# Kernel optimization log

Measured on AMD Instinct MI355X. Metric: run time of the kernel, lower is better.

The kernel has to match this reference:

```python
import jax, jax.numpy as jnp
import numpy as np

HIDDEN = 4096
N_HEADS = 32
N_KV_HEADS = 8
HEAD_DIM = HIDDEN // N_HEADS  # 128
ROPE_THETA = 10000.0
BATCH, SEQ = 2, 2048


def setup_inputs() -> dict:
    key = jax.random.key(0)
    ks = jax.random.split(key, 5)
    s = 0.02
    return {
        "hidden_states": jax.random.normal(ks[0], (BATCH, SEQ, HIDDEN), jnp.float32),
        "position_ids": jnp.broadcast_to(jnp.arange(SEQ, dtype=jnp.int32), (BATCH, SEQ)),
        "Wq": jax.random.normal(ks[1], (HIDDEN, HIDDEN), jnp.float32) * s,
        "Wk": jax.random.normal(ks[2], (N_KV_HEADS * HEAD_DIM, HIDDEN), jnp.float32) * s,
        "Wv": jax.random.normal(ks[3], (N_KV_HEADS * HEAD_DIM, HIDDEN), jnp.float32) * s,
        "Wo": jax.random.normal(ks[4], (HIDDEN, HIDDEN), jnp.float32) * s,
    }


def _rope_cos_sin(position_ids, dtype):
    # HF LlamaRotaryEmbedding: inv_freq over even dims, emb = concat(freqs, freqs)
    inv_freq = 1.0 / (ROPE_THETA ** (jnp.arange(0, HEAD_DIM, 2, dtype=jnp.float32) / HEAD_DIM))
    freqs = position_ids.astype(jnp.float32)[..., None] * inv_freq[None, None, :]  # [B,S,D/2]
    emb = jnp.concatenate([freqs, freqs], axis=-1)  # [B,S,D]
    return jnp.cos(emb).astype(dtype), jnp.sin(emb).astype(dtype)


def _rotate_half(x):
    x1, x2 = jnp.split(x, 2, axis=-1)
    return jnp.concatenate([-x2, x1], axis=-1)


def reference(hidden_states, position_ids, Wq, Wk, Wv, Wo):
    B, S, _ = hidden_states.shape
    dtype = hidden_states.dtype

    # QKV projections (nn.Linear: x @ W.T), reshape to [B, H, S, D]
    q = (hidden_states @ Wq.T).reshape(B, S, N_HEADS, HEAD_DIM).transpose(0, 2, 1, 3)
    k = (hidden_states @ Wk.T).reshape(B, S, N_KV_HEADS, HEAD_DIM).transpose(0, 2, 1, 3)
    v = (hidden_states @ Wv.T).reshape(B, S, N_KV_HEADS, HEAD_DIM).transpose(0, 2, 1, 3)

    # RoPE
    cos, sin = _rope_cos_sin(position_ids, dtype)  # [B,S,D]
    cos_b, sin_b = cos[:, None, :, :], sin[:, None, :, :]
    q = q * cos_b + _rotate_half(q) * sin_b
    k = k * cos_b + _rotate_half(k) * sin_b

    # GQA: group queries over shared kv heads instead of materializing repeat_kv
    groups = N_HEADS // N_KV_HEADS
    qg = q.reshape(B, N_KV_HEADS, groups, S, HEAD_DIM)

    scale = 1.0 / jnp.sqrt(jnp.asarray(HEAD_DIM, dtype=jnp.float32)).astype(dtype)
    scores = jnp.einsum('bkgqd,bkld->bkgql', qg, k) * scale  # [B,KV,G,S,S]

    causal = jnp.tril(jnp.ones((S, S), dtype=bool))
    scores = jnp.where(causal[None, None, None], scores, jnp.asarray(-jnp.inf, scores.dtype))
    probs = jax.nn.softmax(scores.astype(jnp.float32), axis=-1).astype(dtype)

    out = jnp.einsum('bkgql,bkld->bkgqd', probs, v)  # [B,KV,G,S,D]
    out = out.reshape(B, N_HEADS, S, HEAD_DIM).transpose(0, 2, 1, 3).reshape(B, S, HIDDEN)
    return out @ Wo.T
```

## Files before the change

### kernel.cpp

```cpp
#include <hip/hip_runtime.h>
#include <cstdint>
#include <cstddef>

typedef unsigned short u16;
typedef short bf16x8 __attribute__((ext_vector_type(8)));
typedef float f32x4 __attribute__((ext_vector_type(4)));

#define HIDDEN 4096
#define NH 32
#define NKV 8
#define HD 128
#define SEQL 2048
#define BATCH 2
#define NTOK (BATCH*SEQL)
#define QKVN (HIDDEN + 2*NKV*HD)

#define QKS 136

__device__ __forceinline__ u16 f2bf(float f){
    unsigned u = __float_as_uint(f);
    u += 0x7FFF + ((u >> 16) & 1);
    return (u16)(u >> 16);
}
__device__ __forceinline__ float bf2f(u16 h){
    return __uint_as_float(((unsigned)h) << 16);
}
__device__ __forceinline__ f32x4 zero4(){
    f32x4 z; z[0]=0.f; z[1]=0.f; z[2]=0.f; z[3]=0.f; return z;
}

typedef const unsigned int __attribute__((address_space(1)))* gas1_t;
typedef unsigned int __attribute__((address_space(3)))* las3_t;
__device__ __forceinline__ void gload_lds16(const u16* g, u16* l){
    __builtin_amdgcn_global_load_lds((gas1_t)g, (las3_t)l, 16, 0, 0);
}

__global__ __launch_bounds__(256) void cvt_kernel(const float* __restrict__ src,
                                                  u16* __restrict__ dst, int n4){
    int i = blockIdx.x * 256 + threadIdx.x;
    if (i < n4){
        float4 v = ((const float4*)src)[i];
        ushort4 o;
        o.x = f2bf(v.x); o.y = f2bf(v.y); o.z = f2bf(v.z); o.w = f2bf(v.w);
        ((ushort4*)dst)[i] = o;
    }
}

template<int OUT_BF16>
__global__ __launch_bounds__(256) void gemm_bt(const u16* __restrict__ A,
                                               const u16* __restrict__ B,
                                               void* __restrict__ Cp,
                                               int M, int N, int K){
    __shared__ __align__(16) u16 As[128*32];
    __shared__ __align__(16) u16 Bs[128*32];
    int tid = threadIdx.x;
    int wave = tid >> 6, lane = tid & 63, quad = lane >> 4, l16 = lane & 15;
    int wm = wave & 1, wn = wave >> 1;
    size_t row0 = (size_t)blockIdx.y * 128, col0 = (size_t)blockIdx.x * 128;

    f32x4 acc[4][4];
    #pragma unroll
    for (int i=0;i<4;i++)
        #pragma unroll
        for (int j=0;j<4;j++) acc[i][j] = zero4();

    int sg = tid >> 3, ss = tid & 7;
    int scc = ss ^ (sg & 7);
    int sr = sg * 2 + (scc >> 2), sc = scc & 3;
    const u16* Ag = A + (row0 + sr) * (size_t)K + sc * 8;
    const u16* Bg = B + (col0 + sr) * (size_t)K + sc * 8;
    u16* Asp = As + tid * 8;
    u16* Bsp = Bs + tid * 8;
    size_t skip = (size_t)64 * K;

    int fs = (((l16 & 1) * 4 + quad) ^ ((l16 >> 1) & 7)) * 8;
    int aoff = wm * 2048 + (l16 >> 1) * 64 + fs;
    int boff = wn * 2048 + (l16 >> 1) * 64 + fs;

    for (int k0 = 0; k0 < K; k0 += 32){
        gload_lds16(Ag + k0,        Asp);
        gload_lds16(Ag + k0 + skip, Asp + 2048);
        gload_lds16(Bg + k0,        Bsp);
        gload_lds16(Bg + k0 + skip, Bsp + 2048);
        __syncthreads();
        bf16x8 af[4], bfr[4];
        #pragma unroll
        for (int i=0;i<4;i++) af[i]  = *(const bf16x8*)(As + aoff + i*512);
        #pragma unroll
        for (int j=0;j<4;j++) bfr[j] = *(const bf16x8*)(Bs + boff + j*512);
        #pragma unroll
        for (int i=0;i<4;i++)
            #pragma unroll
            for (int j=0;j<4;j++)
                acc[i][j] = __builtin_amdgcn_mfma_f32_16x16x32_bf16(af[i], bfr[j], acc[i][j], 0, 0, 0);
        __syncthreads();
    }

    #pragma unroll
    for (int i=0;i<4;i++)
        #pragma unroll
        for (int j=0;j<4;j++){
            size_t row = row0 + wm*64 + i*16 + quad*4;
            size_t col = col0 + wn*64 + j*16 + l16;
            #pragma unroll
            for (int r=0;r<4;r++){
                if (OUT_BF16) ((u16*)Cp)[(row + r) * (size_t)N + col] = f2bf(acc[i][j][r]);
                else          ((float*)Cp)[(row + r) * (size_t)N + col] = acc[i][j][r];
            }
        }
}

__global__ __launch_bounds__(256) void rope_kernel(u16* __restrict__ qkv,
                                                   const int* __restrict__ pos_ids){
    int idx = blockIdx.x * 256 + threadIdx.x;
    if (idx < 8388608){
        int tok = idx >> 11;
        int rem = idx & 2047;
        int h = rem >> 6, d = rem & 63;
        size_t base = (size_t)tok * QKVN + h * 128 + d;
        float v1 = bf2f(qkv[base]), v2 = bf2f(qkv[base + 64]);
        float p = (float)pos_ids[tok];
        float invf = exp2f((float)d * -0.2076205059304601f);
        float fr = p * invf;
        float s, c; __sincosf(fr, &s, &c);
        qkv[base]      = f2bf(v1 * c - v2 * s);
        qkv[base + 64] = f2bf(v2 * c + v1 * s);
    } else {
        int i2 = idx - 8388608;
        int tok = i2 >> 9;
        int rem = i2 & 511;
        int kv = rem >> 6, d = rem & 63;
        size_t base = (size_t)tok * QKVN + HIDDEN + kv * 128 + d;
        float v1 = bf2f(qkv[base]), v2 = bf2f(qkv[base + 64]);
        float p = (float)pos_ids[tok];
        float invf = exp2f((float)d * -0.2076205059304601f);
        float fr = p * invf;
        float s, c; __sincosf(fr, &s, &c);
        qkv[base]      = f2bf(v1 * c - v2 * s);
        qkv[base + 64] = f2bf(v2 * c + v1 * s);
    }
}

__global__ __launch_bounds__(256) void vtrans_kernel(const u16* __restrict__ qkv,
                                                     u16* __restrict__ Vt){
    int blk = blockIdx.x;
    int tt = blk & 31, bkv = blk >> 5;
    int b = bkv >> 3, kv = bkv & 7;
    const u16* src = qkv + (size_t)(b * SEQL + tt * 64) * QKVN + 5120 + kv * HD;
    u16* dst = Vt + ((size_t)(b * NKV + kv)) * HD * SEQL + tt * 64;
    int tid = threadIdx.x;
    for (int i = tid; i < 1024; i += 256){
        int d = i >> 3, sc = i & 7;
        u16 tmp[8];
        #pragma unroll
        for (int j = 0; j < 8; j++) tmp[j] = src[(size_t)(sc * 8 + j) * QKVN + d];
        *(uint4*)(dst + (size_t)d * SEQL + sc * 8) = *(const uint4*)tmp;
    }
}

__global__ __launch_bounds__(256) void attn_kernel(const u16* __restrict__ qkv,
                                                   const u16* __restrict__ Vt,
                                                   u16* __restrict__ outb){
    __shared__ __align__(16) u16 Ks[64*128];
    __shared__ __align__(16) u16 Vs[128*64];
    __shared__ __align__(16) u16 Ps[4][16*QKS];

    int qt = 31 - (blockIdx.x >> 6);
    int bh = blockIdx.x & 63;
    int h  = bh & 31;
    int b  = bh >> 5;
    int kvh = h >> 2;
    int tid = threadIdx.x, wave = tid >> 6, lane = tid & 63;
    int quad = lane >> 4, l16 = lane & 15;
    int q0 = qt * 64, qrow = q0 + wave * 16;

    const u16* Qg  = qkv + (size_t)(b * SEQL + qrow + l16) * QKVN + h * HD;
    const u16* Kg0 = qkv + (size_t)(b * SEQL) * QKVN + HIDDEN + kvh * HD;
    const u16* Vg  = Vt + ((size_t)(b * NKV + kvh)) * HD * SEQL;
    u16* Pw = &Ps[wave][0];

    const float scale = 0.08838834764831845f;
    bf16x8 qf[4];
    #pragma unroll
    for (int c = 0; c < 4; c++){
        bf16x8 q = *(const bf16x8*)(Qg + c * 32 + quad * 8);
        #pragma unroll
        for (int e = 0; e < 8; e++){
            float f = bf2f((u16)q[e]) * scale;
            q[e] = (short)f2bf(f);
        }
        qf[c] = q;
    }

    const u16* kg[4]; u16* kd[4];
    const u16* vg[4]; u16* vd[4];
    {
        int r4 = lane >> 4, s16 = lane & 15;
        int r8 = lane >> 3, s8 = lane & 7;
        #pragma unroll
        for (int i = 0; i < 4; i++){
            int lr = wave * 16 + i * 4 + r4;
            int cK = s16 ^ (lr & 15);
            kg[i] = Kg0 + (size_t)lr * QKVN + cK * 8;
            kd[i] = Ks + lr * 128 + s16 * 8;
            int dr = wave * 32 + i * 8 + r8;
            int cV = s8 ^ (dr & 7);
            vg[i] = Vg + (size_t)dr * SEQL + cV * 8;
            vd[i] = Vs + dr * 64 + s8 * 8;
        }
    }

    float m_i[4] = {-INFINITY, -INFINITY, -INFINITY, -INFINITY};
    float l_i[4] = {0.f, 0.f, 0.f, 0.f};
    f32x4 Oacc[8];
    #pragma unroll
    for (int t=0;t<8;t++) Oacc[t] = zero4();

    int kend = q0 + 64;
    size_t kOffK = 0;
    for (int k0 = 0; k0 < kend; k0 += 64, kOffK += (size_t)64 * QKVN){
        __syncthreads();
        #pragma unroll
        for (int i = 0; i < 4; i++) gload_lds16(kg[i] + kOffK, kd[i]);
        #pragma unroll
        for (int i = 0; i < 4; i++) gload_lds16(vg[i] + k0, vd[i]);
        __syncthreads();

        f32x4 st[4];
        #pragma unroll
        for (int t=0;t<4;t++) st[t] = zero4();
        #pragma unroll
        for (int c4 = 0; c4 < 4; c4++){
            int cw = c4 * 4 + quad;
            #pragma unroll
            for (int t = 0; t < 4; t++){
                bf16x8 bk = *(const bf16x8*)(Ks + (t*16 + l16)*128 + (cw ^ l16)*8);
                st[t] = __builtin_amdgcn_mfma_f32_16x16x32_bf16(qf[c4], bk, st[t], 0, 0, 0);
            }
        }

        bool needmask = (k0 + 63 >= qrow);
        int row_g = qrow + quad * 4;
        float alpha[4];
        #pragma unroll
        for (int r=0;r<4;r++){
            float mx = m_i[r];
            #pragma unroll
            for (int t=0;t<4;t++){
                float v = st[t][r];
                if (needmask){
                    int col = k0 + t*16 + l16;
                    v = (col <= row_g + r) ? v : -INFINITY;
                }
                st[t][r] = v;
                mx = fmaxf(mx, v);
            }
            #pragma unroll
            for (int m=8;m>=1;m>>=1) mx = fmaxf(mx, __shfl_xor(mx, m));
            float mnew = mx;
            alpha[r] = __expf(m_i[r] - mnew);
            float rs = 0.f;
            #pragma unroll
            for (int t=0;t<4;t++){
                float pv = __expf(st[t][r] - mnew);
                st[t][r] = pv;
                rs += pv;
            }
            #pragma unroll
            for (int m=8;m>=1;m>>=1) rs += __shfl_xor(rs, m);
            l_i[r] = l_i[r] * alpha[r] + rs;
            m_i[r] = mnew;
        }

        #pragma unroll
        for (int t=0;t<8;t++)
            #pragma unroll
            for (int r=0;r<4;r++) Oacc[t][r] *= alpha[r];

        #pragma unroll
        for (int t=0;t<4;t++)
            #pragma unroll
            for (int r=0;r<4;r++)
                Pw[(quad*4 + r)*QKS + t*16 + l16] = f2bf(st[t][r]);

        #pragma unroll
        for (int c2 = 0; c2 < 2; c2++){
            bf16x8 ap = *(const bf16x8*)(Pw + l16*QKS + c2*32 + quad*8);
            int cw = c2 * 4 + quad;
            #pragma unroll
            for (int t = 0; t < 8; t++){
                int d = t*16 + l16;
                bf16x8 bv = *(const bf16x8*)(Vs + d*64 + (cw ^ (l16 & 7))*8);
                Oacc[t] = __builtin_amdgcn_mfma_f32_16x16x32_bf16(ap, bv, Oacc[t], 0, 0, 0);
            }
        }
    }

    float invl[4];
    #pragma unroll
    for (int r=0;r<4;r++) invl[r] = 1.f / l_i[r];
    int row0 = qrow + quad * 4;
    #pragma unroll
    for (int t=0;t<8;t++)
        #pragma unroll
        for (int r=0;r<4;r++){
            size_t o = ((size_t)(b * SEQL + row0 + r)) * HIDDEN + h * HD + t*16 + l16;
            outb[o] = f2bf(Oacc[t][r] * invl[r]);
        }
}

extern "C" void kernel_launch(void* const* d_in, const int* in_sizes, int n_in,
                              void* d_out, int out_size, void* d_ws, size_t ws_size,
                              hipStream_t stream){
    (void)in_sizes; (void)n_in; (void)out_size; (void)ws_size;
    const float* hs  = (const float*)d_in[0];
    const int*   pos = (const int*)d_in[1];
    const float* Wq  = (const float*)d_in[2];
    const float* Wk  = (const float*)d_in[3];
    const float* Wv  = (const float*)d_in[4];
    const float* Wo  = (const float*)d_in[5];
    float* out = (float*)d_out;
    char* ws = (char*)d_ws;

    u16* Xbf  = (u16*)(ws);
    u16* Wqkv = (u16*)(ws + 33554432);
    u16* Wob  = (u16*)(ws + 83886080);
    u16* QKVb = (u16*)(ws + 117440512);
    u16* Vt   = (u16*)(ws + 167772160);
    u16* attn_bf = Xbf;

    cvt_kernel<<<16384, 256, 0, stream>>>(hs, Xbf, 4194304);
    cvt_kernel<<<16384, 256, 0, stream>>>(Wq, Wqkv, 4194304);
    cvt_kernel<<<4096,  256, 0, stream>>>(Wk, Wqkv + (size_t)4096*4096, 1048576);
    cvt_kernel<<<4096,  256, 0, stream>>>(Wv, Wqkv + (size_t)5120*4096, 1048576);
    cvt_kernel<<<16384, 256, 0, stream>>>(Wo, Wob, 4194304);

    gemm_bt<1><<<dim3(48, 32), 256, 0, stream>>>(Xbf, Wqkv, QKVb, NTOK, QKVN, HIDDEN);
    rope_kernel<<<40960, 256, 0, stream>>>(QKVb, pos);
    vtrans_kernel<<<512, 256, 0, stream>>>(QKVb, Vt);
    attn_kernel<<<BATCH*NH*(SEQL/64), 256, 0, stream>>>(QKVb, Vt, attn_bf);
    gemm_bt<0><<<dim3(32, 32), 256, 0, stream>>>(attn_bf, Wob, out, NTOK, HIDDEN, HIDDEN);
}
```

Baseline: 918.2 us.

## Replace GEMM with 256x256-tile 8-wave double-buffered pipelined kernel

Replaces the 128x128, single-buffered, K=32-step GEMM with a 512-thread kernel that computes 256x256 output tiles over K=64 steps. It double-buffers LDS and interleaves global-to-LDS prefetch of the next tiles with MFMA phases, using explicit waitcnt, barriers and setprio. It also remaps block IDs across 8 groups, likely for XCD-aware L2 locality. The aim is to raise arithmetic intensity and hide load latency in both projection GEMMs, at the cost of 128KB of LDS and more registers per block, which lowers occupancy.

```diff
diff --git a/kernel.cpp b/kernel.cpp
--- a/kernel.cpp
+++ b/kernel.cpp
@@ -47,65 +47,109 @@
 }
 
 template<int OUT_BF16>
-__global__ __launch_bounds__(256) void gemm_bt(const u16* __restrict__ A,
-                                               const u16* __restrict__ B,
-                                               void* __restrict__ Cp,
-                                               int M, int N, int K){
-    __shared__ __align__(16) u16 As[128*32];
-    __shared__ __align__(16) u16 Bs[128*32];
+__global__ __launch_bounds__(512) void gemm8_bt(const u16* __restrict__ A,
+                                                const u16* __restrict__ B,
+                                                void* __restrict__ Cp,
+                                                int M, int N, int K){
+    __shared__ __align__(16) u16 L[2][2][256*64];
     int tid = threadIdx.x;
     int wave = tid >> 6, lane = tid & 63, quad = lane >> 4, l16 = lane & 15;
-    int wm = wave & 1, wn = wave >> 1;
-    size_t row0 = (size_t)blockIdx.y * 128, col0 = (size_t)blockIdx.x * 128;
-
-    f32x4 acc[4][4];
-    #pragma unroll
-    for (int i=0;i<4;i++)
+    int wm = wave >> 2, wn = wave & 3;
+
+    int nwg = gridDim.x;
+    int cpx = nwg >> 3;
+    int orig = blockIdx.x;
+    int wg = (orig & 7) * cpx + (orig >> 3);
+    int nbx = N >> 8;
+    int bx = wg % nbx, by = wg / nbx;
+    size_t row0 = (size_t)by * 256, col0 = (size_t)bx * 256;
+
+    int r0 = tid >> 3, cc = (tid & 7) ^ (r0 & 7);
+    const u16* aS0 = A + (row0 + r0) * (size_t)K + cc * 8;
+    const u16* bS0 = B + (col0 + r0) * (size_t)K + cc * 8;
+    u16* ldsd = &L[0][0][0] + tid * 8;
+
+#define STAGE_HALF(mat, half, bufi, kt) do {                                        \
+        const u16* g_ = ((mat) ? bS0 : aS0) + (size_t)((half)*128) * K + (size_t)(kt) * 64; \
+        u16* d_ = ldsd + (bufi)*32768 + (mat)*16384 + (half)*8192;                  \
+        gload_lds16(g_, d_);                                                        \
+        gload_lds16(g_ + (size_t)64 * K, d_ + 4096);                                \
+    } while(0)
+
+    const int nt = K >> 6;
+
+    int swz0 = ((0*4 + quad) ^ (l16 & 7)) * 8;
+    int swz1 = ((1*4 + quad) ^ (l16 & 7)) * 8;
+
+    f32x4 acc[8][4];
+    #pragma unroll
+    for (int i=0;i<8;i++)
         #pragma unroll
         for (int j=0;j<4;j++) acc[i][j] = zero4();
 
-    int sg = tid >> 3, ss = tid & 7;
-    int scc = ss ^ (sg & 7);
-    int sr = sg * 2 + (scc >> 2), sc = scc & 3;
-    const u16* Ag = A + (row0 + sr) * (size_t)K + sc * 8;
-    const u16* Bg = B + (col0 + sr) * (size_t)K + sc * 8;
-    u16* Asp = As + tid * 8;
-    u16* Bsp = Bs + tid * 8;
-    size_t skip = (size_t)64 * K;
-
-    int fs = (((l16 & 1) * 4 + quad) ^ ((l16 >> 1) & 7)) * 8;
-    int aoff = wm * 2048 + (l16 >> 1) * 64 + fs;
-    int boff = wn * 2048 + (l16 >> 1) * 64 + fs;
-
-    for (int k0 = 0; k0 < K; k0 += 32){
-        gload_lds16(Ag + k0,        Asp);
-        gload_lds16(Ag + k0 + skip, Asp + 2048);
-        gload_lds16(Bg + k0,        Bsp);
-        gload_lds16(Bg + k0 + skip, Bsp + 2048);
-        __syncthreads();
-        bf16x8 af[4], bfr[4];
-        #pragma unroll
-        for (int i=0;i<4;i++) af[i]  = *(const bf16x8*)(As + aoff + i*512);
-        #pragma unroll
-        for (int j=0;j<4;j++) bfr[j] = *(const bf16x8*)(Bs + boff + j*512);
-        #pragma unroll
-        for (int i=0;i<4;i++)
-            #pragma unroll
-            for (int j=0;j<4;j++)
-                acc[i][j] = __builtin_amdgcn_mfma_f32_16x16x32_bf16(af[i], bfr[j], acc[i][j], 0, 0, 0);
-        __syncthreads();
-    }
-
-    #pragma unroll
-    for (int i=0;i<4;i++)
-        #pragma unroll
-        for (int j=0;j<4;j++){
-            size_t row = row0 + wm*64 + i*16 + quad*4;
-            size_t col = col0 + wn*64 + j*16 + l16;
-            #pragma unroll
-            for (int r=0;r<4;r++){
-                if (OUT_BF16) ((u16*)Cp)[(row + r) * (size_t)N + col] = f2bf(acc[i][j][r]);
-                else          ((float*)Cp)[(row + r) * (size_t)N + col] = acc[i][j][r];
+    STAGE_HALF(1,0,0,0); STAGE_HALF(1,1,0,0);
+    STAGE_HALF(0,0,0,0); STAGE_HALF(0,1,0,0);
+    STAGE_HALF(1,0,1,1); STAGE_HALF(1,1,1,1);
+
+    bf16x8 bF[4][2];
+    for (int t = 0; t < nt; ++t){
+        if (t < nt - 1) asm volatile("s_waitcnt vmcnt(4)" ::: "memory");
+        else            asm volatile("s_waitcnt vmcnt(0)" ::: "memory");
+        __builtin_amdgcn_s_barrier();
+        const u16* bufA = &L[t & 1][0][0];
+        const u16* bufB = &L[t & 1][1][0];
+
+        #pragma unroll
+        for (int p = 0; p < 4; ++p){
+            bf16x8 aF[2][2];
+            if (p == 0){
+                #pragma unroll
+                for (int ni = 0; ni < 4; ++ni){
+                    int rb = (wn*64 + ni*16 + l16) * 64;
+                    bF[ni][0] = *(const bf16x8*)(bufB + rb + swz0);
+                    bF[ni][1] = *(const bf16x8*)(bufB + rb + swz1);
+                }
+            }
+            #pragma unroll
+            for (int i = 0; i < 2; ++i){
+                int ra = (wm*128 + p*32 + i*16 + l16) * 64;
+                aF[i][0] = *(const bf16x8*)(bufA + ra + swz0);
+                aF[i][1] = *(const bf16x8*)(bufA + ra + swz1);
+            }
+            if (p == 0){ if (t + 1 < nt) STAGE_HALF(0, 0, (t+1)&1, t+1); }
+            if (p == 1){ if (t + 1 < nt) STAGE_HALF(0, 1, (t+1)&1, t+1); }
+            if (p == 2){ if (t + 2 < nt) STAGE_HALF(1, 0, t&1, t+2); }
+            if (p == 3){ if (t + 2 < nt) STAGE_HALF(1, 1, t&1, t+2); }
+
+            __builtin_amdgcn_sched_barrier(0);
+            __builtin_amdgcn_s_barrier();
+            __builtin_amdgcn_sched_barrier(0);
+            __builtin_amdgcn_s_setprio(1);
+            #pragma unroll
+            for (int ni = 0; ni < 4; ++ni)
+                #pragma unroll
+                for (int i = 0; i < 2; ++i){
+                    acc[p*2+i][ni] = __builtin_amdgcn_mfma_f32_16x16x32_bf16(aF[i][0], bF[ni][0], acc[p*2+i][ni], 0, 0, 0);
+                    acc[p*2+i][ni] = __builtin_amdgcn_mfma_f32_16x16x32_bf16(aF[i][1], bF[ni][1], acc[p*2+i][ni], 0, 0, 0);
+                }
+            __builtin_amdgcn_s_setprio(0);
+            __builtin_amdgcn_sched_barrier(0);
+            asm volatile("s_waitcnt lgkmcnt(0)" ::: "memory");
+            if (p < 3) __builtin_amdgcn_s_barrier();
+        }
+    }
+#undef STAGE_HALF
+
+    #pragma unroll
+    for (int mi = 0; mi < 8; ++mi)
+        #pragma unroll
+        for (int ni = 0; ni < 4; ++ni){
+            size_t row = row0 + wm*128 + mi*16 + quad*4;
+            size_t col = col0 + wn*64 + ni*16 + l16;
+            #pragma unroll
+            for (int r = 0; r < 4; ++r){
+                if (OUT_BF16) ((u16*)Cp)[(row + r) * (size_t)N + col] = f2bf(acc[mi][ni][r]);
+                else          ((float*)Cp)[(row + r) * (size_t)N + col] = acc[mi][ni][r];
             }
         }
 }
@@ -335,9 +379,9 @@
     cvt_kernel<<<4096,  256, 0, stream>>>(Wv, Wqkv + (size_t)5120*4096, 1048576);
     cvt_kernel<<<16384, 256, 0, stream>>>(Wo, Wob, 4194304);
 
-    gemm_bt<1><<<dim3(48, 32), 256, 0, stream>>>(Xbf, Wqkv, QKVb, NTOK, QKVN, HIDDEN);
+    gemm8_bt<1><<<384, 512, 0, stream>>>(Xbf, Wqkv, QKVb, NTOK, QKVN, HIDDEN);
     rope_kernel<<<40960, 256, 0, stream>>>(QKVb, pos);
     vtrans_kernel<<<512, 256, 0, stream>>>(QKVb, Vt);
     attn_kernel<<<BATCH*NH*(SEQL/64), 256, 0, stream>>>(QKVb, Vt, attn_bf);
-    gemm_bt<0><<<dim3(32, 32), 256, 0, stream>>>(attn_bf, Wob, out, NTOK, HIDDEN, HIDDEN);
-}
+    gemm8_bt<0><<<256, 512, 0, stream>>>(attn_bf, Wob, out, NTOK, HIDDEN, HIDDEN);
+}
```

Result: faster. 803.8 us (-12.5%).
